# Performance work log

Measured on AMD Instinct MI355X. Metric: run time of the kernel, lower is better.

Reference implementation:

```python
import jax, jax.numpy as jnp
import numpy as np

B, S, IN, OUT, P = 4, 1024, 128, 128, 16
CTX = min(IN, OUT)
MAX_SEQ = 4096


def setup_inputs() -> dict:
    key = jax.random.key(0)
    keys = iter(jax.random.split(key, 32))
    nk = lambda: next(keys)

    def linear(fi, fo):
        lim = 1.0 / np.sqrt(fi)
        W = jax.random.uniform(nk(), (fi, fo), jnp.float32, -lim, lim)
        b = jax.random.uniform(nk(), (fo,), jnp.float32, -lim, lim)
        return W, b

    x = jax.random.normal(nk(), (B, S, IN), jnp.float32)
    context_features = jax.random.normal(nk(), (B, S, CTX), jnp.float32)
    flow_patterns = jax.random.normal(nk(), (P, OUT, IN), jnp.float32) * 0.1
    w_sel1, b_sel1 = linear(IN + CTX, 2 * P)
    w_sel2, b_sel2 = linear(2 * P, P)
    w_int1, b_int1 = linear(IN + CTX, 64)
    w_int2, b_int2 = linear(64, 1)
    w_win1, b_win1 = linear(IN, 64)
    w_win2, b_win2 = linear(64, 1)
    return dict(x=x, context_features=context_features, flow_patterns=flow_patterns,
                w_sel1=w_sel1, b_sel1=b_sel1, w_sel2=w_sel2, b_sel2=b_sel2,
                w_int1=w_int1, b_int1=b_int1, w_int2=w_int2, b_int2=b_int2,
                w_win1=w_win1, b_win1=b_win1, w_win2=w_win2, b_win2=b_win2)


def _gelu(v):
    return jax.nn.gelu(v, approximate=False)  # torch nn.GELU default (erf)


def reference(x, context_features, flow_patterns,
              w_sel1, b_sel1, w_sel2, b_sel2,
              w_int1, b_int1, w_int2, b_int2,
              w_win1, b_win1, w_win2, b_win2):
    # combined input [B,S,IN+CTX]
    combined = jnp.concatenate([x, context_features], axis=-1)
    # pattern weights [B,S,P]
    pattern_weights = jax.nn.softmax(_gelu(combined @ w_sel1 + b_sel1) @ w_sel2 + b_sel2, axis=-1)
    # per-token flow matrix [B,S,OUT,IN]
    flow = jnp.einsum('bsp,poi->bsoi', pattern_weights, flow_patterns)
    # flow intensity [B,S,1] -> [B,S,1,1]
    intensity = jax.nn.sigmoid(_gelu(combined @ w_int1 + b_int1) @ w_int2 + b_int2)
    flow = flow * intensity[..., None]
    # adaptive window size [B,1]
    window_size = jax.nn.sigmoid(_gelu(x.mean(axis=1) @ w_win1 + b_win1) @ w_win2 + b_win2)
    window_size = window_size * (MAX_SEQ - 256) + 256
    # context-aware topk sparsity over flattened out*in dim
    adaptive_sparsity = 0.1 * jnp.mean(window_size / MAX_SEQ)  # scalar
    D = OUT * IN
    k = jnp.maximum(1, jnp.floor(D * adaptive_sparsity)).astype(jnp.int32)
    flat = flow.reshape(B, S, D)
    a = jnp.abs(flat)
    sorted_a = jnp.sort(a, axis=-1)  # ascending
    # k-th largest abs value per (b,s) row; k is a traced scalar -> dynamic_slice
    thr = jax.lax.dynamic_slice_in_dim(sorted_a, D - k, 1, axis=-1)  # [B,S,1]
    mask = jax.lax.stop_gradient((a >= thr).astype(flat.dtype))
    return (mask * flat).reshape(B, S, OUT, IN)
```

## Files before the change

kernel.cpp:

```cpp
#include <hip/hip_runtime.h>
#include <math.h>

#define S_   1024
#define D_   16384
#define CAPL 512
#define NB   512

typedef float v4f __attribute__((ext_vector_type(4)));

__device__ __forceinline__ double gelu64(double v) {
    return 0.5 * v * (1.0 + erf(v * 0.70710678118654752440));
}
__device__ __forceinline__ double sigmoid64(double z) {
    return 1.0 / (1.0 + exp(-z));
}
__device__ __forceinline__ float rfl(float x) {
    return __uint_as_float(__builtin_amdgcn_readfirstlane(__float_as_uint(x)));
}

__global__ __launch_bounds__(256) void mlp_kernel(
    const float* __restrict__ x, const float* __restrict__ ctx,
    const float* __restrict__ w_sel1, const float* __restrict__ b_sel1,
    const float* __restrict__ w_sel2, const float* __restrict__ b_sel2,
    const float* __restrict__ w_int1, const float* __restrict__ b_int1,
    const float* __restrict__ w_int2, const float* __restrict__ b_int2,
    double* __restrict__ pw64, float* __restrict__ pw32,
    double* __restrict__ it64, float* __restrict__ it32)
{
    __shared__ double comb[2][256];
    __shared__ double h1[2][32];
    __shared__ double ipart[2][2];
    const int tid = threadIdx.x;
    const int tok0 = blockIdx.x * 2;
    const int t = tid >> 7, local = tid & 127;

    for (int r = 0; r < 2; ++r) {
        int idx = tid + r * 256;
        int tk = idx >> 8, i = idx & 255;
        comb[tk][i] = (double)((i < 128) ? x[(tok0 + tk) * 128 + i]
                                         : ctx[(tok0 + tk) * 128 + (i - 128)]);
    }
    __syncthreads();

    {
        int u = local >> 2, sl = local & 3;
        int i0 = sl * 64;
        double s0 = (sl == 0) ? (double)b_sel1[u] : 0.0, s1 = 0.0;
        for (int i = 0; i < 64; i += 2) {
            s0 = fma(comb[t][i0 + i],     (double)w_sel1[(i0 + i) * 32 + u],     s0);
            s1 = fma(comb[t][i0 + i + 1], (double)w_sel1[(i0 + i + 1) * 32 + u], s1);
        }
        double s = s0 + s1;
        s += __shfl_xor(s, 1);
        s += __shfl_xor(s, 2);
        if (sl == 0) h1[t][u] = gelu64(s);
    }
    {
        int u = local >> 1, sl = local & 1;
        int i0 = sl * 128;
        double a0 = (sl == 0) ? (double)b_int1[u] : 0.0, a1 = 0.0, a2 = 0.0, a3 = 0.0;
        for (int i = 0; i < 128; i += 4) {
            a0 = fma(comb[t][i0 + i],     (double)w_int1[(i0 + i) * 64 + u],     a0);
            a1 = fma(comb[t][i0 + i + 1], (double)w_int1[(i0 + i + 1) * 64 + u], a1);
            a2 = fma(comb[t][i0 + i + 2], (double)w_int1[(i0 + i + 2) * 64 + u], a2);
            a3 = fma(comb[t][i0 + i + 3], (double)w_int1[(i0 + i + 3) * 64 + u], a3);
        }
        double s = (a0 + a1) + (a2 + a3);
        s += __shfl_xor(s, 1);
        double val = (sl == 0) ? gelu64(s) * (double)w_int2[u] : 0.0;
        for (int off = 2; off <= 32; off <<= 1)
            val += __shfl_xor(val, off);
        val += __shfl_xor(val, 1);
        if ((local & 63) == 0) ipart[t][local >> 6] = val;
    }
    __syncthreads();

    if (tid < 32) {
        int t2 = tid >> 4, u = tid & 15;
        double z = (double)b_sel2[u];
        for (int j = 0; j < 32; ++j)
            z = fma(h1[t2][j], (double)w_sel2[j * 16 + u], z);
        double m = z;
        for (int off = 8; off >= 1; off >>= 1) m = fmax(m, __shfl_xor(m, off));
        double e = exp(z - m);
        double ssum = e;
        for (int off = 8; off >= 1; off >>= 1) ssum += __shfl_xor(ssum, off);
        double pwv = e / ssum;
        pw64[(tok0 + t2) * 16 + u] = pwv;
        pw32[(tok0 + t2) * 16 + u] = (float)pwv;
    } else if (tid < 34) {
        int t3 = tid - 32;
        double iv = sigmoid64(ipart[t3][0] + ipart[t3][1] + (double)b_int2[0]);
        it64[tok0 + t3] = iv;
        it32[tok0 + t3] = (float)iv;
    }
}

__global__ __launch_bounds__(256) void win_part_kernel(
    const float* __restrict__ x, double* __restrict__ wpart)
{
    __shared__ double red[2][128];
    const int tid = threadIdx.x;
    const int b = blockIdx.x >> 4, chunk = blockIdx.x & 15;
    int i = tid & 127, h = tid >> 7;
    double a0 = 0.0, a1 = 0.0;
    int s0 = b * S_ + chunk * 64 + h * 32;
    for (int j = 0; j < 32; j += 2) {
        a0 += (double)x[(s0 + j) * 128 + i];
        a1 += (double)x[(s0 + j + 1) * 128 + i];
    }
    red[h][i] = a0 + a1;
    __syncthreads();
    if (tid < 128)
        wpart[(b * 16 + chunk) * 128 + tid] = red[0][tid] + red[1][tid];
}

__global__ __launch_bounds__(256) void win_fin_kernel(
    const double* __restrict__ wpart,
    const float* __restrict__ w_win1, const float* __restrict__ b_win1,
    const float* __restrict__ w_win2, const float* __restrict__ b_win2,
    double* __restrict__ win_out)
{
    __shared__ double xm[4][128];
    const int tid = threadIdx.x;
    const int b = tid >> 6, lane = tid & 63;
    for (int r = 0; r < 2; ++r) {
        int i = lane + r * 64;
        double s = 0.0;
        for (int c = 0; c < 16; ++c)
            s += wpart[(b * 16 + c) * 128 + i];
        xm[b][i] = s * (1.0 / 1024.0);
    }
    __syncthreads();
    {
        int u = lane;
        double s0 = (double)b_win1[u], s1 = 0.0;
        for (int i = 0; i < 128; i += 2) {
            s0 = fma(xm[b][i],     (double)w_win1[i * 64 + u],       s0);
            s1 = fma(xm[b][i + 1], (double)w_win1[(i + 1) * 64 + u], s1);
        }
        double c = gelu64(s0 + s1) * (double)w_win2[u];
        for (int off = 32; off >= 1; off >>= 1) c += __shfl_xor(c, off);
        if (lane == 0)
            win_out[b] = sigmoid64(c + (double)b_win2[0]) * 3840.0 + 256.0;
    }
}

__global__ __launch_bounds__(512, 4) void flow_kernel(
    const float* __restrict__ patterns,
    const double* __restrict__ pw64, const float* __restrict__ pw32,
    const double* __restrict__ it64, const float* __restrict__ it32,
    const double* __restrict__ win,
    float* __restrict__ out)
{
    __shared__ unsigned hist[2][NB];
    __shared__ unsigned flagBits[2][512];
    __shared__ unsigned listIdx[2][CAPL];
    __shared__ double listVal[2][CAPL];
    __shared__ float smax[2][8];
    __shared__ int sred[8];
    __shared__ int bcastB[2];
    __shared__ unsigned listCnt[2];

    const int tid = threadIdx.x;
    const int lane = tid & 63, wv = tid >> 6;
    const int t0 = blockIdx.x * 2, t1 = t0 + 1;

    for (int r = tid; r < 2 * NB; r += 512) hist[r >> 9][r & (NB - 1)] = 0;
    for (int r = tid; r < 1024; r += 512) flagBits[r >> 9][r & 511] = 0;
    if (tid < 2) listCnt[tid] = 0;

    double w0 = win[0] * (1.0 / 4096.0), w1 = win[1] * (1.0 / 4096.0);
    double w2 = win[2] * (1.0 / 4096.0), w3 = win[3] * (1.0 / 4096.0);
    double mean = (((w0 + w1) + w2) + w3) * 0.25;
    double kd = floor(16384.0 * (0.1 * mean));
    int k = (kd < 1.0) ? 1 : (int)kd;

    float qw0[16], qw1[16];
#pragma unroll
    for (int p = 0; p < 16; ++p) {
        qw0[p] = rfl(pw32[t0 * 16 + p]);
        qw1[p] = rfl(pw32[t1 * 16 + p]);
    }
    float i0 = rfl(it32[t0]), i1 = rfl(it32[t1]);

    const v4f* pat4 = (const v4f*)patterns;
    v4f v0[8], v1[8];
#pragma unroll
    for (int c = 0; c < 8; ++c) {
        int grp = c * 512 + tid;
        v4f a0 = (v4f)(0.0f), a1 = (v4f)(0.0f);
#pragma unroll
        for (int p = 0; p < 16; ++p) {
            v4f pp = pat4[p * 4096 + grp];
            a0 += qw0[p] * pp;
            a1 += qw1[p] * pp;
        }
        v0[c] = a0 * i0;
        v1[c] = a1 * i1;
    }

    float mx0 = 0.0f, mx1 = 0.0f;
#pragma unroll
    for (int c = 0; c < 8; ++c) {
        mx0 = fmaxf(mx0, fmaxf(fmaxf(fabsf(v0[c].x), fabsf(v0[c].y)),
                               fmaxf(fabsf(v0[c].z), fabsf(v0[c].w))));
        mx1 = fmaxf(mx1, fmaxf(fmaxf(fabsf(v1[c].x), fabsf(v1[c].y)),
                               fmaxf(fabsf(v1[c].z), fabsf(v1[c].w))));
    }
    for (int off = 32; off >= 1; off >>= 1) {
        mx0 = fmaxf(mx0, __shfl_xor(mx0, off));
        mx1 = fmaxf(mx1, __shfl_xor(mx1, off));
    }
    if (lane == 0) { smax[0][wv] = mx0; smax[1][wv] = mx1; }
    __syncthreads();
    mx0 = smax[0][0]; mx1 = smax[1][0];
#pragma unroll
    for (int w = 1; w < 8; ++w) {
        mx0 = fmaxf(mx0, smax[0][w]);
        mx1 = fmaxf(mx1, smax[1][w]);
    }
    int base0 = (int)(__float_as_uint(mx0) >> 17) - (NB - 1);
    int base1 = (int)(__float_as_uint(mx1) >> 17) - (NB - 1);
    if (base0 < 0) base0 = 0;
    if (base1 < 0) base1 = 0;

#pragma unroll
    for (int c = 0; c < 8; ++c) {
#pragma unroll
        for (int q = 0; q < 4; ++q) {
            int b0 = (int)(__float_as_uint(fabsf(v0[c][q])) >> 17) - base0;
            if (b0 > 0) atomicAdd(&hist[0][b0 > NB - 1 ? NB - 1 : b0], 1u);
            int b1 = (int)(__float_as_uint(fabsf(v1[c][q])) >> 17) - base1;
            if (b1 > 0) atomicAdd(&hist[1][b1 > NB - 1 ? NB - 1 : b1], 1u);
        }
    }
    __syncthreads();

    if (wv < 2) {
        int t = wv;
        int sum8 = 0;
#pragma unroll
        for (int j = 0; j < 8; ++j) sum8 += (int)hist[t][lane * 8 + j];
        int suffix = sum8;
        for (int off = 1; off <= 32; off <<= 1) {
            int other = __shfl_down(suffix, off);
            if (lane + off < 64) suffix += other;
        }
        int sufNext = __shfl_down(suffix, 1);
        if (lane == 63) sufNext = 0;
        unsigned long long msk = __ballot(suffix >= k);
        int Lstar = (msk == 0) ? 0 : (63 - __clzll(msk));
        if (lane == Lstar) {
            int cnt = sufNext, B = Lstar * 8;
            for (int j = 7; j >= 0; --j) {
                cnt += (int)hist[t][Lstar * 8 + j];
                if (cnt >= k) { B = Lstar * 8 + j; break; }
            }
            bcastB[t] = B;
        }
    }
    __syncthreads();

    int B0 = bcastB[0], B1 = bcastB[1];
    float loF0 = (B0 + base0) ? __uint_as_float((unsigned)(B0 + base0) << 17) : 0.0f;
    float hiF0 = __uint_as_float((unsigned)(B0 + base0 + 1) << 17);
    float loF1 = (B1 + base1) ? __uint_as_float((unsigned)(B1 + base1) << 17) : 0.0f;
    float hiF1 = __uint_as_float((unsigned)(B1 + base1 + 1) << 17);

    float E0 = 3e-6f * i0, E1 = 3e-6f * i1;
    float loCut0 = loF0 - 2.0f * E0, hiCut0 = hiF0 + 2.0f * E0;
    float loCut1 = loF1 - 2.0f * E1, hiCut1 = hiF1 + 2.0f * E1;

    int ns0 = 0, ns1 = 0;
#pragma unroll
    for (int c = 0; c < 8; ++c) {
#pragma unroll
        for (int q = 0; q < 4; ++q) {
            unsigned e = (unsigned)(4 * (c * 512 + tid) + q);
            float a0 = fabsf(v0[c][q]);
            if (a0 >= hiCut0) ns0++;
            else if (a0 >= loCut0) {
                unsigned pos = atomicAdd(&listCnt[0], 1u);
                if (pos < CAPL) listIdx[0][pos] = e;
            }
            float a1 = fabsf(v1[c][q]);
            if (a1 >= hiCut1) ns1++;
            else if (a1 >= loCut1) {
                unsigned pos = atomicAdd(&listCnt[1], 1u);
                if (pos < CAPL) listIdx[1][pos] = e;
            }
        }
    }
    {
        int pk = ns0 | (ns1 << 16);
#pragma unroll
        for (int off = 32; off >= 1; off >>= 1) pk += __shfl_xor(pk, off);
        if (lane == 0) sred[wv] = pk;
    }
    __syncthreads();
    int tot = 0;
#pragma unroll
    for (int w = 0; w < 8; ++w) tot += sred[w];
    int m0 = k - (tot & 0xffff), m1 = k - (tot >> 16);
    int c0n = (int)(listCnt[0] < CAPL ? listCnt[0] : CAPL);
    int c1n = (int)(listCnt[1] < CAPL ? listCnt[1] : CAPL);

    double itt0 = it64[t0], itt1 = it64[t1];
    int totL = c0n + c1n;
    for (int g = tid; g < totL; g += 512) {
        int tk = (g >= c0n);
        int e = tk ? (g - c0n) : g;
        unsigned idx = listIdx[tk][e];
        const double* pwp = pw64 + (tk ? t1 : t0) * 16;
        double s = 0.0;
#pragma unroll
        for (int p = 0; p < 16; ++p)
            s = fma(pwp[p], (double)patterns[p * D_ + idx], s);
        listVal[tk][e] = fabs(s * (tk ? itt1 : itt0));
    }
    __syncthreads();
    for (int g = tid; g < totL; g += 512) {
        int tk = (g >= c0n);
        int e = tk ? (g - c0n) : g;
        double my = listVal[tk][e];
        int cnt = tk ? c1n : c0n, m = tk ? m1 : m0;
        int r = 0;
        for (int j = 0; j < cnt; ++j) r += (listVal[tk][j] > my);
        if (r < m) {
            unsigned idx = listIdx[tk][e];
            atomicOr(&flagBits[tk][idx >> 5], 1u << (idx & 31));
        }
    }
    __syncthreads();

    v4f* o0p = (v4f*)(out + (size_t)t0 * D_);
    v4f* o1p = (v4f*)(out + (size_t)t1 * D_);
#pragma unroll
    for (int c = 0; c < 8; ++c) {
        int grp = c * 512 + tid;
        v4f r0, r1;
#pragma unroll
        for (int q = 0; q < 4; ++q) {
            unsigned e = (unsigned)(4 * grp + q);
            float av = fabsf(v0[c][q]);
            bool keep = (av >= hiCut0);
            if (!keep && av >= loCut0) keep = (flagBits[0][e >> 5] >> (e & 31)) & 1u;
            r0[q] = keep ? v0[c][q] : 0.0f;
            av = fabsf(v1[c][q]);
            keep = (av >= hiCut1);
            if (!keep && av >= loCut1) keep = (flagBits[1][e >> 5] >> (e & 31)) & 1u;
            r1[q] = keep ? v1[c][q] : 0.0f;
        }
        __builtin_nontemporal_store(r0, &o0p[grp]);
        __builtin_nontemporal_store(r1, &o1p[grp]);
    }
}

extern "C" void kernel_launch(void* const* d_in, const int* in_sizes, int n_in,
                              void* d_out, int out_size, void* d_ws, size_t ws_size,
                              hipStream_t stream) {
    const float* x        = (const float*)d_in[0];
    const float* ctx      = (const float*)d_in[1];
    const float* patterns = (const float*)d_in[2];
    const float* w_sel1   = (const float*)d_in[3];
    const float* b_sel1   = (const float*)d_in[4];
    const float* w_sel2   = (const float*)d_in[5];
    const float* b_sel2   = (const float*)d_in[6];
    const float* w_int1   = (const float*)d_in[7];
    const float* b_int1   = (const float*)d_in[8];
    const float* w_int2   = (const float*)d_in[9];
    const float* b_int2   = (const float*)d_in[10];
    const float* w_win1   = (const float*)d_in[11];
    const float* b_win1   = (const float*)d_in[12];
    const float* w_win2   = (const float*)d_in[13];
    const float* b_win2   = (const float*)d_in[14];

    double* ws    = (double*)d_ws;
    double* win   = ws;
    double* pw64  = ws + 8;
    double* it64  = pw64 + 65536;
    double* wpart = it64 + 4096;
    float*  pw32  = (float*)(wpart + 8192);
    float*  it32  = pw32 + 65536;
    float*  out   = (float*)d_out;

    hipLaunchKernelGGL(mlp_kernel, dim3(2048), dim3(256), 0, stream,
                       x, ctx, w_sel1, b_sel1, w_sel2, b_sel2,
                       w_int1, b_int1, w_int2, b_int2, pw64, pw32, it64, it32);
    hipLaunchKernelGGL(win_part_kernel, dim3(64), dim3(256), 0, stream, x, wpart);
    hipLaunchKernelGGL(win_fin_kernel, dim3(1), dim3(256), 0, stream,
                       wpart, w_win1, b_win1, w_win2, b_win2, win);
    hipLaunchKernelGGL(flow_kernel, dim3(2048), dim3(512), 0, stream,
                       patterns, pw64, pw32, it64, it32, win, out);
}
```

Baseline: 445.2 us.

## Process four tokens per 1024-thread flow block to reuse pattern loads

The flow kernel now handles four tokens per block with 1024 threads instead of two tokens with 512, so each pattern vector load feeds four accumulators. This halves pattern-matrix reads per token and doubles per-block shared memory for histograms, lists and flags. The strong-count reduction is now done twice: once in a packed form whose result is overwritten, then again with a per-token loop containing extra barriers. Register pressure rises with 64 weights and 16 value vectors per thread, and the larger block may lower occupancy.

Result: slower. 1.326 ms (+197.9%).

```diff
diff --git a/kernel.cpp b/kernel.cpp
--- a/kernel.cpp
+++ b/kernel.cpp
@@ -146,29 +146,29 @@
     }
 }
 
-__global__ __launch_bounds__(512, 4) void flow_kernel(
+__global__ __launch_bounds__(1024, 4) void flow_kernel(
     const float* __restrict__ patterns,
     const double* __restrict__ pw64, const float* __restrict__ pw32,
     const double* __restrict__ it64, const float* __restrict__ it32,
     const double* __restrict__ win,
     float* __restrict__ out)
 {
-    __shared__ unsigned hist[2][NB];
-    __shared__ unsigned flagBits[2][512];
-    __shared__ unsigned listIdx[2][CAPL];
-    __shared__ double listVal[2][CAPL];
-    __shared__ float smax[2][8];
-    __shared__ int sred[8];
-    __shared__ int bcastB[2];
-    __shared__ unsigned listCnt[2];
+    __shared__ unsigned hist[4][NB];
+    __shared__ unsigned flagBits[4][512];
+    __shared__ unsigned listIdx[4][CAPL];
+    __shared__ double listVal[4][CAPL];
+    __shared__ float smax[4][16];
+    __shared__ int sred[16];
+    __shared__ int bcastB[4];
+    __shared__ unsigned listCnt[4];
 
     const int tid = threadIdx.x;
     const int lane = tid & 63, wv = tid >> 6;
-    const int t0 = blockIdx.x * 2, t1 = t0 + 1;
-
-    for (int r = tid; r < 2 * NB; r += 512) hist[r >> 9][r & (NB - 1)] = 0;
-    for (int r = tid; r < 1024; r += 512) flagBits[r >> 9][r & 511] = 0;
-    if (tid < 2) listCnt[tid] = 0;
+    const int t0 = blockIdx.x * 4;
+
+    for (int r = tid; r < 4 * NB; r += 1024) hist[r >> 9][r & (NB - 1)] = 0;
+    for (int r = tid; r < 2048; r += 1024) flagBits[r >> 9][r & 511] = 0;
+    if (tid < 4) listCnt[tid] = 0;
 
     double w0 = win[0] * (1.0 / 4096.0), w1 = win[1] * (1.0 / 4096.0);
     double w2 = win[2] * (1.0 / 4096.0), w3 = win[3] * (1.0 / 4096.0);
@@ -176,68 +176,74 @@
     double kd = floor(16384.0 * (0.1 * mean));
     int k = (kd < 1.0) ? 1 : (int)kd;
 
-    float qw0[16], qw1[16];
-#pragma unroll
-    for (int p = 0; p < 16; ++p) {
-        qw0[p] = rfl(pw32[t0 * 16 + p]);
-        qw1[p] = rfl(pw32[t1 * 16 + p]);
-    }
-    float i0 = rfl(it32[t0]), i1 = rfl(it32[t1]);
+    float qw[4][16], it[4];
+#pragma unroll
+    for (int t = 0; t < 4; ++t) {
+#pragma unroll
+        for (int p = 0; p < 16; ++p)
+            qw[t][p] = rfl(pw32[(t0 + t) * 16 + p]);
+        it[t] = rfl(it32[t0 + t]);
+    }
 
     const v4f* pat4 = (const v4f*)patterns;
-    v4f v0[8], v1[8];
-#pragma unroll
-    for (int c = 0; c < 8; ++c) {
-        int grp = c * 512 + tid;
-        v4f a0 = (v4f)(0.0f), a1 = (v4f)(0.0f);
+    v4f v[4][4];
+#pragma unroll
+    for (int c = 0; c < 4; ++c) {
+        int grp = c * 1024 + tid;
+        v4f a0 = (v4f)(0.0f), a1 = (v4f)(0.0f), a2 = (v4f)(0.0f), a3 = (v4f)(0.0f);
 #pragma unroll
         for (int p = 0; p < 16; ++p) {
             v4f pp = pat4[p * 4096 + grp];
-            a0 += qw0[p] * pp;
-            a1 += qw1[p] * pp;
-        }
-        v0[c] = a0 * i0;
-        v1[c] = a1 * i1;
-    }
-
-    float mx0 = 0.0f, mx1 = 0.0f;
-#pragma unroll
-    for (int c = 0; c < 8; ++c) {
-        mx0 = fmaxf(mx0, fmaxf(fmaxf(fabsf(v0[c].x), fabsf(v0[c].y)),
-                               fmaxf(fabsf(v0[c].z), fabsf(v0[c].w))));
-        mx1 = fmaxf(mx1, fmaxf(fmaxf(fabsf(v1[c].x), fabsf(v1[c].y)),
-                               fmaxf(fabsf(v1[c].z), fabsf(v1[c].w))));
-    }
-    for (int off = 32; off >= 1; off >>= 1) {
-        mx0 = fmaxf(mx0, __shfl_xor(mx0, off));
-        mx1 = fmaxf(mx1, __shfl_xor(mx1, off));
-    }
-    if (lane == 0) { smax[0][wv] = mx0; smax[1][wv] = mx1; }
-    __syncthreads();
-    mx0 = smax[0][0]; mx1 = smax[1][0];
-#pragma unroll
-    for (int w = 1; w < 8; ++w) {
-        mx0 = fmaxf(mx0, smax[0][w]);
-        mx1 = fmaxf(mx1, smax[1][w]);
-    }
-    int base0 = (int)(__float_as_uint(mx0) >> 17) - (NB - 1);
-    int base1 = (int)(__float_as_uint(mx1) >> 17) - (NB - 1);
-    if (base0 < 0) base0 = 0;
-    if (base1 < 0) base1 = 0;
-
-#pragma unroll
-    for (int c = 0; c < 8; ++c) {
-#pragma unroll
-        for (int q = 0; q < 4; ++q) {
-            int b0 = (int)(__float_as_uint(fabsf(v0[c][q])) >> 17) - base0;
-            if (b0 > 0) atomicAdd(&hist[0][b0 > NB - 1 ? NB - 1 : b0], 1u);
-            int b1 = (int)(__float_as_uint(fabsf(v1[c][q])) >> 17) - base1;
-            if (b1 > 0) atomicAdd(&hist[1][b1 > NB - 1 ? NB - 1 : b1], 1u);
-        }
-    }
-    __syncthreads();
-
-    if (wv < 2) {
+            a0 += qw[0][p] * pp;
+            a1 += qw[1][p] * pp;
+            a2 += qw[2][p] * pp;
+            a3 += qw[3][p] * pp;
+        }
+        v[0][c] = a0 * it[0];
+        v[1][c] = a1 * it[1];
+        v[2][c] = a2 * it[2];
+        v[3][c] = a3 * it[3];
+    }
+
+    float mx[4];
+#pragma unroll
+    for (int t = 0; t < 4; ++t) {
+        float m = 0.0f;
+#pragma unroll
+        for (int c = 0; c < 4; ++c)
+            m = fmaxf(m, fmaxf(fmaxf(fabsf(v[t][c].x), fabsf(v[t][c].y)),
+                               fmaxf(fabsf(v[t][c].z), fabsf(v[t][c].w))));
+        for (int off = 32; off >= 1; off >>= 1)
+            m = fmaxf(m, __shfl_xor(m, off));
+        if (lane == 0) smax[t][wv] = m;
+        mx[t] = m;
+    }
+    __syncthreads();
+    int base[4];
+#pragma unroll
+    for (int t = 0; t < 4; ++t) {
+        float m = smax[t][0];
+#pragma unroll
+        for (int w = 1; w < 16; ++w) m = fmaxf(m, smax[t][w]);
+        mx[t] = m;
+        int b = (int)(__float_as_uint(m) >> 17) - (NB - 1);
+        base[t] = (b < 0) ? 0 : b;
+    }
+
+#pragma unroll
+    for (int t = 0; t < 4; ++t) {
+#pragma unroll
+        for (int c = 0; c < 4; ++c) {
+#pragma unroll
+            for (int q = 0; q < 4; ++q) {
+                int b = (int)(__float_as_uint(fabsf(v[t][c][q])) >> 17) - base[t];
+                if (b > 0) atomicAdd(&hist[t][b > NB - 1 ? NB - 1 : b], 1u);
+            }
+        }
+    }
+    __syncthreads();
+
+    if (wv < 4) {
         int t = wv;
         int sum8 = 0;
 #pragma unroll
@@ -262,98 +268,124 @@
     }
     __syncthreads();
 
-    int B0 = bcastB[0], B1 = bcastB[1];
-    float loF0 = (B0 + base0) ? __uint_as_float((unsigned)(B0 + base0) << 17) : 0.0f;
-    float hiF0 = __uint_as_float((unsigned)(B0 + base0 + 1) << 17);
-    float loF1 = (B1 + base1) ? __uint_as_float((unsigned)(B1 + base1) << 17) : 0.0f;
-    float hiF1 = __uint_as_float((unsigned)(B1 + base1 + 1) << 17);
-
-    float E0 = 3e-6f * i0, E1 = 3e-6f * i1;
-    float loCut0 = loF0 - 2.0f * E0, hiCut0 = hiF0 + 2.0f * E0;
-    float loCut1 = loF1 - 2.0f * E1, hiCut1 = hiF1 + 2.0f * E1;
-
-    int ns0 = 0, ns1 = 0;
-#pragma unroll
-    for (int c = 0; c < 8; ++c) {
-#pragma unroll
-        for (int q = 0; q < 4; ++q) {
-            unsigned e = (unsigned)(4 * (c * 512 + tid) + q);
-            float a0 = fabsf(v0[c][q]);
-            if (a0 >= hiCut0) ns0++;
-            else if (a0 >= loCut0) {
-                unsigned pos = atomicAdd(&listCnt[0], 1u);
-                if (pos < CAPL) listIdx[0][pos] = e;
-            }
-            float a1 = fabsf(v1[c][q]);
-            if (a1 >= hiCut1) ns1++;
-            else if (a1 >= loCut1) {
-                unsigned pos = atomicAdd(&listCnt[1], 1u);
-                if (pos < CAPL) listIdx[1][pos] = e;
-            }
-        }
-    }
+    float loCut[4], hiCut[4];
+#pragma unroll
+    for (int t = 0; t < 4; ++t) {
+        int B = bcastB[t];
+        float loF = (B + base[t]) ? __uint_as_float((unsigned)(B + base[t]) << 17) : 0.0f;
+        float hiF = __uint_as_float((unsigned)(B + base[t] + 1) << 17);
+        float E = 3e-6f * it[t];
+        loCut[t] = loF - 2.0f * E;
+        hiCut[t] = hiF + 2.0f * E;
+    }
+
+    int nsPack = 0;
+#pragma unroll
+    for (int t = 0; t < 4; ++t) {
+        int ns = 0;
+#pragma unroll
+        for (int c = 0; c < 4; ++c) {
+#pragma unroll
+            for (int q = 0; q < 4; ++q) {
+                unsigned e = (unsigned)(4 * (c * 1024 + tid) + q);
+                float a = fabsf(v[t][c][q]);
+                if (a >= hiCut[t]) ns++;
+                else if (a >= loCut[t]) {
+                    unsigned pos = atomicAdd(&listCnt[t], 1u);
+                    if (pos < CAPL) listIdx[t][pos] = e;
+                }
+            }
+        }
+        nsPack |= ns << (8 * t);
+    }
+#pragma unroll
+    for (int off = 32; off >= 1; off >>= 1) nsPack += __shfl_xor(nsPack, off);
+    if (lane == 0) sred[wv] = nsPack;
+    __syncthreads();
+    int m[4], cn[4];
     {
-        int pk = ns0 | (ns1 << 16);
-#pragma unroll
-        for (int off = 32; off >= 1; off >>= 1) pk += __shfl_xor(pk, off);
-        if (lane == 0) sred[wv] = pk;
-    }
-    __syncthreads();
-    int tot = 0;
-#pragma unroll
-    for (int w = 0; w < 8; ++w) tot += sred[w];
-    int m0 = k - (tot & 0xffff), m1 = k - (tot >> 16);
-    int c0n = (int)(listCnt[0] < CAPL ? listCnt[0] : CAPL);
-    int c1n = (int)(listCnt[1] < CAPL ? listCnt[1] : CAPL);
-
-    double itt0 = it64[t0], itt1 = it64[t1];
-    int totL = c0n + c1n;
-    for (int g = tid; g < totL; g += 512) {
-        int tk = (g >= c0n);
-        int e = tk ? (g - c0n) : g;
-        unsigned idx = listIdx[tk][e];
-        const double* pwp = pw64 + (tk ? t1 : t0) * 16;
-        double s = 0.0;
-#pragma unroll
-        for (int p = 0; p < 16; ++p)
-            s = fma(pwp[p], (double)patterns[p * D_ + idx], s);
-        listVal[tk][e] = fabs(s * (tk ? itt1 : itt0));
-    }
-    __syncthreads();
-    for (int g = tid; g < totL; g += 512) {
-        int tk = (g >= c0n);
-        int e = tk ? (g - c0n) : g;
-        double my = listVal[tk][e];
-        int cnt = tk ? c1n : c0n, m = tk ? m1 : m0;
-        int r = 0;
-        for (int j = 0; j < cnt; ++j) r += (listVal[tk][j] > my);
-        if (r < m) {
-            unsigned idx = listIdx[tk][e];
-            atomicOr(&flagBits[tk][idx >> 5], 1u << (idx & 31));
-        }
-    }
-    __syncthreads();
-
-    v4f* o0p = (v4f*)(out + (size_t)t0 * D_);
-    v4f* o1p = (v4f*)(out + (size_t)t1 * D_);
-#pragma unroll
-    for (int c = 0; c < 8; ++c) {
-        int grp = c * 512 + tid;
-        v4f r0, r1;
-#pragma unroll
-        for (int q = 0; q < 4; ++q) {
-            unsigned e = (unsigned)(4 * grp + q);
-            float av = fabsf(v0[c][q]);
-            bool keep = (av >= hiCut0);
-            if (!keep && av >= loCut0) keep = (flagBits[0][e >> 5] >> (e & 31)) & 1u;
-            r0[q] = keep ? v0[c][q] : 0.0f;
-            av = fabsf(v1[c][q]);
-            keep = (av >= hiCut1);
-            if (!keep && av >= loCut1) keep = (flagBits[1][e >> 5] >> (e & 31)) & 1u;
-            r1[q] = keep ? v1[c][q] : 0.0f;
-        }
-        __builtin_nontemporal_store(r0, &o0p[grp]);
-        __builtin_nontemporal_store(r1, &o1p[grp]);
+        int tot0 = 0, tot1 = 0, tot2 = 0, tot3 = 0;
+#pragma unroll
+        for (int w = 0; w < 16; ++w) {
+            int s = sred[w];
+            tot0 += (s)       & 0x3ff;
+            tot1 += (s >> 8)  & 0x3ff;
+            tot2 += (s >> 16) & 0x3ff;
+            tot3 += (s >> 24) & 0xff;
+        }
+        m[0] = tot0; m[1] = tot1; m[2] = tot2; m[3] = tot3;
+    }
+    {
+#pragma unroll
+        for (int t = 0; t < 4; ++t) {
+            int ns = 0;
+#pragma unroll
+            for (int c = 0; c < 4; ++c) {
+#pragma unroll
+                for (int q = 0; q < 4; ++q)
+                    ns += (fabsf(v[t][c][q]) >= hiCut[t]);
+            }
+#pragma unroll
+            for (int off = 32; off >= 1; off >>= 1) ns += __shfl_xor(ns, off);
+            if (lane == 0) sred[wv] = ns;
+            __syncthreads();
+            int tot = 0;
+#pragma unroll
+            for (int w = 0; w < 16; ++w) tot += sred[w];
+            m[t] = k - tot;
+            __syncthreads();
+        }
+    }
+#pragma unroll
+    for (int t = 0; t < 4; ++t)
+        cn[t] = (int)(listCnt[t] < CAPL ? listCnt[t] : CAPL);
+
+#pragma unroll
+    for (int t = 0; t < 4; ++t) {
+        if (tid < cn[t]) {
+            unsigned idx = listIdx[t][tid];
+            const double* pwp = pw64 + (size_t)(t0 + t) * 16;
+            double itt = it64[t0 + t];
+            double s = 0.0;
+#pragma unroll
+            for (int p = 0; p < 16; ++p)
+                s = fma(pwp[p], (double)patterns[p * D_ + idx], s);
+            listVal[t][tid] = fabs(s * itt);
+        }
+    }
+    __syncthreads();
+#pragma unroll
+    for (int t = 0; t < 4; ++t) {
+        if (tid < cn[t]) {
+            double my = listVal[t][tid];
+            int r = 0;
+            for (int j = 0; j < cn[t]; ++j) r += (listVal[t][j] > my);
+            if (r < m[t]) {
+                unsigned idx = listIdx[t][tid];
+                atomicOr(&flagBits[t][idx >> 5], 1u << (idx & 31));
+            }
+        }
+    }
+    __syncthreads();
+
+#pragma unroll
+    for (int t = 0; t < 4; ++t) {
+        v4f* op = (v4f*)(out + (size_t)(t0 + t) * D_);
+#pragma unroll
+        for (int c = 0; c < 4; ++c) {
+            int grp = c * 1024 + tid;
+            v4f r;
+#pragma unroll
+            for (int q = 0; q < 4; ++q) {
+                unsigned e = (unsigned)(4 * grp + q);
+                float av = fabsf(v[t][c][q]);
+                bool keep = (av >= hiCut[t]);
+                if (!keep && av >= loCut[t])
+                    keep = (flagBits[t][e >> 5] >> (e & 31)) & 1u;
+                r[q] = keep ? v[t][c][q] : 0.0f;
+            }
+            __builtin_nontemporal_store(r, &op[grp]);
+        }
     }
 }
 
@@ -391,6 +423,6 @@
     hipLaunchKernelGGL(win_part_kernel, dim3(64), dim3(256), 0, stream, x, wpart);
     hipLaunchKernelGGL(win_fin_kernel, dim3(1), dim3(256), 0, stream,
                        wpart, w_win1, b_win1, w_win2, b_win2, win);
-    hipLaunchKernelGGL(flow_kernel, dim3(2048), dim3(512), 0, stream,
+    hipLaunchKernelGGL(flow_kernel, dim3(1024), dim3(1024), 0, stream,
                        patterns, pw64, pw32, it64, it32, win, out);
 }
```
